# Kernel tuning notes

Hardware: AMD Instinct MI355X
Metric: run time of the kernel (lower is better)

## Reference

```python
import jax, jax.numpy as jnp
import numpy as np

N_NODES = 100000
N_EDGES = 3200000
IN_F = 256
OUT_F = 128


def setup_inputs() -> dict:
    key = jax.random.key(0)
    k1, k2, k3, k4, k5, k6 = jax.random.split(key, 6)
    x = jax.random.normal(k1, (N_NODES, IN_F), dtype=jnp.float32)
    adj_rows = jax.random.randint(k2, (N_EDGES,), 0, N_NODES, dtype=jnp.int32)
    adj_cols = jax.random.randint(k3, (N_EDGES,), 0, N_NODES, dtype=jnp.int32)
    adj_vals = jax.random.uniform(k4, (N_EDGES,), dtype=jnp.float32)
    stdv = 1.0 / np.sqrt(IN_F)
    W = jax.random.uniform(k5, (IN_F, OUT_F), minval=-stdv, maxval=stdv, dtype=jnp.float32)
    b = jax.random.uniform(k6, (OUT_F,), minval=-stdv, maxval=stdv, dtype=jnp.float32)
    return {"x": x, "adj_rows": adj_rows, "adj_cols": adj_cols,
            "adj_vals": adj_vals, "W": W, "b": b}


def reference(x, adj_rows, adj_cols, adj_vals, W, b):
    # support = Linear(x): [N, out]
    support = x @ W + b
    # spmm(adj, support): out[i] = sum_{e: rows[e]==i} vals[e] * support[cols[e]]
    msgs = adj_vals[:, None] * support[adj_cols]  # [E, out]
    out = jax.ops.segment_sum(msgs, adj_rows, num_segments=N_NODES)
    return out
```

## Files before the change

### kernel.cpp

```cpp
#include <hip/hip_runtime.h>
#include <stdint.h>

#define NN 100000
#define NE 3200000
#define KF 256
#define MF 128

#define RB 64
#define NB ((NN + RB - 1) / RB)
#define EPB 16384
#define PTH 1024
#define EPT (EPB / PTH)
#define PGRID ((NE + EPB - 1) / EPB)
#define SCAPB 2560
#define RPT 10

typedef __attribute__((ext_vector_type(8))) short bf16x8;
typedef __attribute__((ext_vector_type(4))) float floatx4;

__device__ __forceinline__ unsigned short f2bf(float f) {
  union { float f; unsigned int i; } w; w.f = f;
  unsigned int u = w.i;
  u += 0x7FFFu + ((u >> 16) & 1u);
  return (unsigned short)(u >> 16);
}

__global__ __launch_bounds__(256) void wt_kernel(const float* __restrict__ W,
                                                 unsigned short* __restrict__ Wt,
                                                 unsigned int* __restrict__ cursor) {
  int idx = blockIdx.x * 256 + threadIdx.x;
  int k = idx >> 7;
  int c = idx & 127;
  Wt[(size_t)c * KF + k] = f2bf(W[(size_t)k * MF + c]);
  if (idx < NB) cursor[idx] = (unsigned int)idx * SCAPB;
}

__global__ __launch_bounds__(256) void gemm_kernel(const float* __restrict__ x,
                                                   const unsigned short* __restrict__ Wt,
                                                   const float* __restrict__ bias,
                                                   unsigned short* __restrict__ support) {
  __shared__ unsigned short Ax[64][72];
  __shared__ unsigned short Wl[128][72];
  const int tid = threadIdx.x;
  const int row0 = blockIdx.x * 64;
  const int lane = tid & 63;
  const int wv = tid >> 6;
  const int m = lane & 15;
  const int quad = lane >> 4;

  floatx4 acc[4][2];
#pragma unroll
  for (int rt = 0; rt < 4; ++rt)
#pragma unroll
    for (int c2 = 0; c2 < 2; ++c2) acc[rt][c2] = (floatx4){0.f, 0.f, 0.f, 0.f};

  for (int kb = 0; kb < 4; ++kb) {
    if (kb) __syncthreads();
#pragma unroll
    for (int i = 0; i < 4; ++i) {
      int u = tid + i * 256;
      int r = u >> 4;
      int q = u & 15;
      float4 v = make_float4(0.f, 0.f, 0.f, 0.f);
      if (row0 + r < NN)
        v = *(const float4*)(x + (size_t)(row0 + r) * KF + kb * 64 + q * 4);
      ushort4 p;
      p.x = f2bf(v.x); p.y = f2bf(v.y); p.z = f2bf(v.z); p.w = f2bf(v.w);
      *(ushort4*)(&Ax[r][q * 4]) = p;
    }
#pragma unroll
    for (int i = 0; i < 4; ++i) {
      int u = tid + i * 256;
      int c = u >> 3;
      int kq = u & 7;
      *(uint4*)(&Wl[c][kq * 8]) = *(const uint4*)(Wt + (size_t)c * KF + kb * 64 + kq * 8);
    }
    __syncthreads();
#pragma unroll
    for (int kc = 0; kc < 2; ++kc) {
      int k0 = kc * 32 + quad * 8;
      bf16x8 af[4];
#pragma unroll
      for (int rt = 0; rt < 4; ++rt)
        af[rt] = *(const bf16x8*)(&Ax[rt * 16 + m][k0]);
#pragma unroll
      for (int c2 = 0; c2 < 2; ++c2) {
        bf16x8 bfv = *(const bf16x8*)(&Wl[(wv * 2 + c2) * 16 + m][k0]);
#pragma unroll
        for (int rt = 0; rt < 4; ++rt)
          acc[rt][c2] = __builtin_amdgcn_mfma_f32_16x16x32_bf16(af[rt], bfv, acc[rt][c2], 0, 0, 0);
      }
    }
  }
#pragma unroll
  for (int c2 = 0; c2 < 2; ++c2) {
    int col = (wv * 2 + c2) * 16 + m;
    float bv = bias[col];
#pragma unroll
    for (int rt = 0; rt < 4; ++rt) {
#pragma unroll
      for (int rg = 0; rg < 4; ++rg) {
        int grow = row0 + rt * 16 + quad * 4 + rg;
        if (grow < NN)
          support[(size_t)grow * MF + col] = f2bf(acc[rt][c2][rg] + bv);
      }
    }
  }
}

__global__ __launch_bounds__(PTH) void part_kernel(const int* __restrict__ rows,
                                                   const int* __restrict__ cols,
                                                   const float* __restrict__ vals,
                                                   unsigned int* __restrict__ cursor,
                                                   uint2* __restrict__ binned) {
  __shared__ unsigned int hist[NB];
  __shared__ unsigned int base[NB];
  const int tid = threadIdx.x;
  const int e0 = blockIdx.x * EPB;
  for (int i = tid; i < NB; i += PTH) hist[i] = 0u;
  __syncthreads();
  unsigned int pk[EPT];
#pragma unroll
  for (int k = 0; k < EPT; ++k) {
    int e = e0 + tid + k * PTH;
    if (e < NE) {
      unsigned int r = (unsigned int)rows[e];
      unsigned int rank = atomicAdd(&hist[r >> 6], 1u);
      pk[k] = r | (rank << 17);
    } else pk[k] = 0xFFFFFFFFu;
  }
  __syncthreads();
  for (int i = tid; i < NB; i += PTH) {
    unsigned int c = hist[i];
    base[i] = c ? atomicAdd(&cursor[i], c) : 0u;
  }
  __syncthreads();
#pragma unroll
  for (int k = 0; k < EPT; ++k) {
    if (pk[k] != 0xFFFFFFFFu) {
      int e = e0 + tid + k * PTH;
      unsigned int r = pk[k] & 0x1FFFFu;
      unsigned int rank = pk[k] >> 17;
      unsigned int b = r >> 6;
      unsigned int pos = base[b] + rank;
      if (pos < (b + 1u) * SCAPB) {
        unsigned int key = ((r & 63u) << 17) | (unsigned int)cols[e];
        binned[pos] = make_uint2(key, __float_as_uint(vals[e]));
      }
    }
  }
}

#define FMA4(ev, sv) { \
    float v_ = __uint_as_float((ev).y); \
    a0 = fmaf(v_, __uint_as_float((sv).x << 16), a0); \
    a1 = fmaf(v_, __uint_as_float((sv).x & 0xFFFF0000u), a1); \
    a2 = fmaf(v_, __uint_as_float((sv).y << 16), a2); \
    a3 = fmaf(v_, __uint_as_float((sv).y & 0xFFFF0000u), a3); \
  }
#define SUP(ev) (*(const uint2*)(support_u + (size_t)(ev).x * 64 + hl * 2))

__global__ __launch_bounds__(256) void sortgather_kernel(const unsigned int* __restrict__ cursor,
                                                         const uint2* __restrict__ binned,
                                                         const unsigned int* __restrict__ support_u,
                                                         float* __restrict__ out) {
  __shared__ uint2 stage[SCAPB];
  __shared__ unsigned int lcnt[RB];
  __shared__ unsigned int lbase[RB + 1];
  const int tid = threadIdx.x;
  const unsigned int start = blockIdx.x * SCAPB;
  unsigned int end = cursor[blockIdx.x];
  if (end > start + SCAPB) end = start + SCAPB;
  if (tid < RB) lcnt[tid] = 0u;
  __syncthreads();
  uint2 rec[RPT];
  unsigned short rk[RPT];
  unsigned short rl_[RPT];
#pragma unroll
  for (int k = 0; k < RPT; ++k) {
    unsigned int i = start + (unsigned int)tid + (unsigned int)k * 256u;
    rec[k] = make_uint2(0u, 0u); rk[k] = 0; rl_[k] = 0xFFFFu;
    if (i < end) {
      rec[k] = binned[i];
      unsigned int rl = rec[k].x >> 17;
      rl_[k] = (unsigned short)rl;
      rk[k] = (unsigned short)atomicAdd(&lcnt[rl], 1u);
    }
  }
  __syncthreads();
  if (tid < 64) {
    unsigned int v = lcnt[tid];
    unsigned int inc = v;
#pragma unroll
    for (int d = 1; d < 64; d <<= 1) {
      unsigned int n = __shfl_up(inc, d, 64);
      if (tid >= d) inc += n;
    }
    lbase[tid] = inc - v;
    if (tid == 63) lbase[64] = inc;
  }
  __syncthreads();
#pragma unroll
  for (int k = 0; k < RPT; ++k) {
    if (rl_[k] != 0xFFFFu) {
      unsigned int pos = lbase[rl_[k]] + (unsigned int)rk[k];
      if (pos < SCAPB) stage[pos] = make_uint2(rec[k].x & 0x1FFFFu, rec[k].y);
    }
  }
  __syncthreads();
  const int lane = tid & 63;
  const int wv = tid >> 6;
  const int half = lane >> 5;
  const int hl = lane & 31;
  const int node0 = blockIdx.x * RB;
#pragma unroll 1
  for (int nn = 0; nn < 16; ++nn) {
    const int rl = wv * 16 + nn;
    const int node = node0 + rl;
    unsigned int i = lbase[rl];
    const unsigned int e = lbase[rl + 1];
    float a0 = 0.f, a1 = 0.f, a2 = 0.f, a3 = 0.f;
    for (; i + 16 <= e; i += 16) {
      unsigned int j = i + half * 8;
      uint2 e0 = stage[j + 0];
      uint2 e1 = stage[j + 1];
      uint2 e2 = stage[j + 2];
      uint2 e3 = stage[j + 3];
      uint2 e4 = stage[j + 4];
      uint2 e5 = stage[j + 5];
      uint2 e6 = stage[j + 6];
      uint2 e7 = stage[j + 7];
      uint2 s0 = SUP(e0);
      uint2 s1 = SUP(e1);
      uint2 s2 = SUP(e2);
      uint2 s3 = SUP(e3);
      uint2 s4 = SUP(e4);
      uint2 s5 = SUP(e5);
      uint2 s6 = SUP(e6);
      uint2 s7 = SUP(e7);
      FMA4(e0, s0); FMA4(e1, s1); FMA4(e2, s2); FMA4(e3, s3);
      FMA4(e4, s4); FMA4(e5, s5); FMA4(e6, s6); FMA4(e7, s7);
    }
    if (i + 8 <= e) {
      unsigned int j = i + half * 4;
      uint2 e0 = stage[j + 0];
      uint2 e1 = stage[j + 1];
      uint2 e2 = stage[j + 2];
      uint2 e3 = stage[j + 3];
      uint2 s0 = SUP(e0);
      uint2 s1 = SUP(e1);
      uint2 s2 = SUP(e2);
      uint2 s3 = SUP(e3);
      FMA4(e0, s0); FMA4(e1, s1); FMA4(e2, s2); FMA4(e3, s3);
      i += 8;
    }
    if (i + 4 <= e) {
      unsigned int j = i + half * 2;
      uint2 e0 = stage[j + 0];
      uint2 e1 = stage[j + 1];
      uint2 s0 = SUP(e0);
      uint2 s1 = SUP(e1);
      FMA4(e0, s0); FMA4(e1, s1);
      i += 4;
    }
    if (i + 2 <= e) {
      uint2 e0 = stage[i + half];
      uint2 s0 = SUP(e0);
      FMA4(e0, s0);
      i += 2;
    }
    if (i < e && half == 0) {
      uint2 e0 = stage[i];
      uint2 s0 = SUP(e0);
      FMA4(e0, s0);
    }
    a0 += __shfl(a0, hl + 32);
    a1 += __shfl(a1, hl + 32);
    a2 += __shfl(a2, hl + 32);
    a3 += __shfl(a3, hl + 32);
    if (half == 0 && node < NN) {
      float4 o = make_float4(a0, a1, a2, a3);
      *(float4*)(out + (size_t)node * MF + hl * 4) = o;
    }
  }
}

extern "C" void kernel_launch(void* const* d_in, const int* in_sizes, int n_in,
                              void* d_out, int out_size, void* d_ws, size_t ws_size,
                              hipStream_t stream) {
  const float* x    = (const float*)d_in[0];
  const int*   rows = (const int*)d_in[1];
  const int*   cols = (const int*)d_in[2];
  const float* vals = (const float*)d_in[3];
  const float* W    = (const float*)d_in[4];
  const float* bias = (const float*)d_in[5];

  char* ws = (char*)d_ws;
  unsigned short* Wt      = (unsigned short*)ws;
  unsigned short* support = (unsigned short*)(ws + 65536);
  uint2*          binned  = (uint2*)(ws + 65536 + 25600000ull);
  unsigned int*   cursor  = (unsigned int*)(ws + 57675776ull);

  wt_kernel<<<128, 256, 0, stream>>>(W, Wt, cursor);
  gemm_kernel<<<(NN + 63) / 64, 256, 0, stream>>>(x, Wt, bias, support);
  part_kernel<<<PGRID, PTH, 0, stream>>>(rows, cols, vals, cursor, binned);
  sortgather_kernel<<<NB, 256, 0, stream>>>(cursor, binned,
                                            (const unsigned int*)support, (float*)d_out);
}
```

Measured before the change: 402.1 us.

## Prefetch next K-slab of x and W into registers during GEMM; halve edges per block

New measurement: 414.0 us. +3.0%, slower.

```diff
diff --git a/kernel.cpp b/kernel.cpp
--- a/kernel.cpp
+++ b/kernel.cpp
@@ -8,7 +8,7 @@
 
 #define RB 64
 #define NB ((NN + RB - 1) / RB)
-#define EPB 16384
+#define EPB 8192
 #define PTH 1024
 #define EPT (EPB / PTH)
 #define PGRID ((NE + EPB - 1) / EPB)
@@ -54,26 +54,54 @@
 #pragma unroll
     for (int c2 = 0; c2 < 2; ++c2) acc[rt][c2] = (floatx4){0.f, 0.f, 0.f, 0.f};
 
+  float4 xr[4];
+  uint4  wr[4];
+#pragma unroll
+  for (int i = 0; i < 4; ++i) {
+    int u = tid + i * 256;
+    int r = u >> 4, q = u & 15;
+    xr[i] = make_float4(0.f, 0.f, 0.f, 0.f);
+    if (row0 + r < NN)
+      xr[i] = *(const float4*)(x + (size_t)(row0 + r) * KF + q * 4);
+  }
+#pragma unroll
+  for (int i = 0; i < 4; ++i) {
+    int u = tid + i * 256;
+    int c = u >> 3, kq = u & 7;
+    wr[i] = *(const uint4*)(Wt + (size_t)c * KF + kq * 8);
+  }
+
   for (int kb = 0; kb < 4; ++kb) {
     if (kb) __syncthreads();
 #pragma unroll
     for (int i = 0; i < 4; ++i) {
       int u = tid + i * 256;
-      int r = u >> 4;
-      int q = u & 15;
-      float4 v = make_float4(0.f, 0.f, 0.f, 0.f);
-      if (row0 + r < NN)
-        v = *(const float4*)(x + (size_t)(row0 + r) * KF + kb * 64 + q * 4);
+      int r = u >> 4, q = u & 15;
       ushort4 p;
-      p.x = f2bf(v.x); p.y = f2bf(v.y); p.z = f2bf(v.z); p.w = f2bf(v.w);
+      p.x = f2bf(xr[i].x); p.y = f2bf(xr[i].y); p.z = f2bf(xr[i].z); p.w = f2bf(xr[i].w);
       *(ushort4*)(&Ax[r][q * 4]) = p;
     }
 #pragma unroll
     for (int i = 0; i < 4; ++i) {
       int u = tid + i * 256;
-      int c = u >> 3;
-      int kq = u & 7;
-      *(uint4*)(&Wl[c][kq * 8]) = *(const uint4*)(Wt + (size_t)c * KF + kb * 64 + kq * 8);
+      int c = u >> 3, kq = u & 7;
+      *(uint4*)(&Wl[c][kq * 8]) = wr[i];
+    }
+    if (kb < 3) {
+#pragma unroll
+      for (int i = 0; i < 4; ++i) {
+        int u = tid + i * 256;
+        int r = u >> 4, q = u & 15;
+        xr[i] = make_float4(0.f, 0.f, 0.f, 0.f);
+        if (row0 + r < NN)
+          xr[i] = *(const float4*)(x + (size_t)(row0 + r) * KF + (kb + 1) * 64 + q * 4);
+      }
+#pragma unroll
+      for (int i = 0; i < 4; ++i) {
+        int u = tid + i * 256;
+        int c = u >> 3, kq = u & 7;
+        wr[i] = *(const uint4*)(Wt + (size_t)c * KF + (kb + 1) * 64 + kq * 8);
+      }
     }
     __syncthreads();
 #pragma unroll
```
